# Performance work log

Hardware: AMD Instinct MI355X
Metric: run time of the kernel (lower is better)

Reference implementation:

```python
import jax, jax.numpy as jnp
import numpy as np

T = 2048          # tokens (flattened prefill)
H = 3584          # hidden_size
NH = 16           # num query heads
NKV = 8           # num kv heads
G = NH // NKV     # GQA group size
D = 256           # head_dim
SCALE = 256.0 ** -0.5   # query_pre_attn_scalar ** -0.5
WINDOW = 1024     # sliding_window_size
CAP = 50.0        # logit softcap
BASE = 10000.0    # rope theta
NEG = -1e30


def _rope(x, positions):
    # x: [T, n, D], neox-style rotary over full head_dim
    half = D // 2
    inv_freq = 1.0 / (BASE ** (jnp.arange(0, D, 2, dtype=jnp.float32) / D))  # [half]
    ang = positions.astype(jnp.float32)[:, None] * inv_freq  # [T, half]
    cos = jnp.cos(ang)[:, None, :]  # [T,1,half]
    sin = jnp.sin(ang)[:, None, :]
    x1, x2 = x[..., :half], x[..., half:]
    return jnp.concatenate([x1 * cos - x2 * sin, x2 * cos + x1 * sin], axis=-1)


def setup_inputs() -> dict:
    key = jax.random.key(0)
    ks = jax.random.split(key, 5)
    s = 0.02
    return {
        "hidden_states": jax.random.normal(ks[0], (T, H), dtype=jnp.float32),
        "Wq": jax.random.normal(ks[1], (H, NH * D), dtype=jnp.float32) * s,
        "Wk": jax.random.normal(ks[2], (H, NKV * D), dtype=jnp.float32) * s,
        "Wv": jax.random.normal(ks[3], (H, NKV * D), dtype=jnp.float32) * s,
        "Wo": jax.random.normal(ks[4], (NH * D, H), dtype=jnp.float32) * s,
        "positions": jnp.arange(T, dtype=jnp.int32),
    }


def reference(hidden_states, Wq, Wk, Wv, Wo, positions):
    q = (hidden_states @ Wq).reshape(T, NH, D)
    k = (hidden_states @ Wk).reshape(T, NKV, D)
    v = (hidden_states @ Wv).reshape(T, NKV, D)
    q = _rope(q, positions)
    k = _rope(k, positions)

    # GQA attention: group query heads over kv heads
    qg = (q * SCALE).reshape(T, NKV, G, D)
    scores = jnp.einsum('qhgd,khd->hgqk', qg, k)  # [NKV,G,T,T]
    scores = CAP * jnp.tanh(scores / CAP)         # logit softcap

    i = jnp.arange(T)[:, None]
    j = jnp.arange(T)[None, :]
    mask = (j <= i) & (i - j < WINDOW)            # causal + sliding window
    scores = jnp.where(mask, scores, NEG)

    p = jax.nn.softmax(scores, axis=-1)
    o = jnp.einsum('hgqk,khd->qhgd', p, v).reshape(T, NH * D)
    return o @ Wo
```

## Files before the change

### kernel.cpp

```cpp
#include <hip/hip_runtime.h>
#include <math.h>

typedef __attribute__((ext_vector_type(8))) __bf16 bf16x8;
typedef __attribute__((ext_vector_type(4))) __bf16 bf16x4;
typedef __attribute__((ext_vector_type(4))) float f32x4;

#define TSEQ 2048
#define HDIM 3584
#define NQH  16
#define NKVH 8
#define DH   256
#define WIN  1024
#define QKD  (NQH * DH)
#define KVD  (NKVH * DH)
#define QLD  8256
#define OLD  4160
#define WOLD 4160
#define VLD  2112

#define MFMA __builtin_amdgcn_mfma_f32_16x16x32_bf16

__device__ __forceinline__ void gload_lds16(const void* g, void* l) {
  __builtin_amdgcn_global_load_lds(
      (const __attribute__((address_space(1))) void*)g,
      (__attribute__((address_space(3))) void*)l, 16, 0, 0);
}


__global__ void cvt_bf16_kernel(const float* __restrict__ in,
                                __bf16* __restrict__ out, long n) {
  long i = ((long)blockIdx.x * blockDim.x + threadIdx.x) * 4;
  if (i >= n) return;
  float4 v = *reinterpret_cast<const float4*>(in + i);
  bf16x4 o4;
  o4.x = (__bf16)v.x; o4.y = (__bf16)v.y; o4.z = (__bf16)v.z; o4.w = (__bf16)v.w;
  *reinterpret_cast<bf16x4*>(out + i) = o4;
}

__global__ void transpose_all_kernel(const float* __restrict__ Wq,
                                     const float* __restrict__ Wk,
                                     const float* __restrict__ Wv,
                                     const float* __restrict__ Wo,
                                     __bf16* __restrict__ WqT,
                                     __bf16* __restrict__ WkT,
                                     __bf16* __restrict__ WvT,
                                     __bf16* __restrict__ WoT) {
  __shared__ float tile[64][65];
  int id = blockIdx.x;
  const float* src; __bf16* dst; int R, C, ldo;
  if (id < 3584)      { src = Wq; dst = WqT; R = HDIM; C = QKD; ldo = HDIM; }
  else if (id < 5376) { id -= 3584; src = Wk; dst = WkT; R = HDIM; C = KVD; ldo = HDIM; }
  else if (id < 7168) { id -= 5376; src = Wv; dst = WvT; R = HDIM; C = KVD; ldo = HDIM; }
  else                { id -= 7168; src = Wo; dst = WoT; R = QKD; C = HDIM; ldo = WOLD; }
  const int nbx = C >> 6;
  const int c0 = (id % nbx) * 64, r0 = (id / nbx) * 64;
  const int tid = threadIdx.x;
#pragma unroll
  for (int it = 0; it < 4; ++it) {
    int f = tid + it * 256;
    int row = f >> 4, c4 = (f & 15) * 4;
    float4 v = *reinterpret_cast<const float4*>(&src[(size_t)(r0 + row) * C + c0 + c4]);
    tile[row][c4] = v.x; tile[row][c4 + 1] = v.y;
    tile[row][c4 + 2] = v.z; tile[row][c4 + 3] = v.w;
  }
  __syncthreads();
#pragma unroll
  for (int it = 0; it < 2; ++it) {
    int s = tid + it * 256;
    int oc = s >> 3, rb = (s & 7) * 8;
    bf16x8 o8;
#pragma unroll
    for (int j = 0; j < 8; ++j) o8[j] = (__bf16)tile[rb + j][oc];
    *reinterpret_cast<bf16x8*>(&dst[(size_t)(c0 + oc) * ldo + r0 + rb]) = o8;
  }
}

__global__ void transpose_bf16_kernel(const __bf16* __restrict__ in,
                                      __bf16* __restrict__ out, int ldin, int ldout) {
  __shared__ __bf16 tile[32][33];
  const int tx = threadIdx.x, ty = threadIdx.y;
  const int c0 = blockIdx.x * 32, r0 = blockIdx.y * 32;
#pragma unroll
  for (int i = 0; i < 4; ++i)
    tile[ty + i * 8][tx] = in[(size_t)(r0 + ty + i * 8) * ldin + (c0 + tx)];
  __syncthreads();
#pragma unroll
  for (int i = 0; i < 4; ++i)
    out[(size_t)(c0 + ty + i * 8) * ldout + (r0 + tx)] = tile[tx][ty + i * 8];
}

__global__ void rope_table_kernel(const int* __restrict__ positions,
                                  float* __restrict__ ct,
                                  float* __restrict__ st) {
  int i = blockIdx.x * blockDim.x + threadIdx.x;
  if (i >= TSEQ * 128) return;
  int t = i >> 7, j = i & 127;
  float invf = (float)exp((double)(-2 * j) * (9.210340371976184 / 256.0));
  float ang = (float)positions[t] * invf;
  ct[i] = cosf(ang);
  st[i] = sinf(ang);
}

__global__ void rope_qk_kernel(__bf16* __restrict__ qkv,
                               const float* __restrict__ ct,
                               const float* __restrict__ st) {
  int i = blockIdx.x * blockDim.x + threadIdx.x;
  int jg = (i & 15) * 8;
  int th = i >> 4;
  int t = th / 24;
  int hh = th - t * 24;
  float scale = (hh < 16) ? 0.0625f : 1.0f;
  size_t base = (size_t)t * QLD + ((hh < 16) ? hh * DH : QKD + (hh - 16) * DH) + jg;
  bf16x8 x1 = *reinterpret_cast<const bf16x8*>(qkv + base);
  bf16x8 x2 = *reinterpret_cast<const bf16x8*>(qkv + base + 128);
  const float* cp = ct + (t << 7) + jg;
  const float* sp = st + (t << 7) + jg;
  bf16x8 o1, o2;
#pragma unroll
  for (int e = 0; e < 8; ++e) {
    float c = cp[e], s = sp[e];
    float a = (float)x1[e], b = (float)x2[e];
    o1[e] = (__bf16)((a * c - b * s) * scale);
    o2[e] = (__bf16)((b * c + a * s) * scale);
  }
  *reinterpret_cast<bf16x8*>(qkv + base) = o1;
  *reinterpret_cast<bf16x8*>(qkv + base + 128) = o2;
}


__device__ __forceinline__ void stage_half(const __bf16* __restrict__ gbase,
                                           int row0, int ldg, int k0,
                                           __bf16* lds_half, int tid) {
  const int lane = tid & 63;
  const int w = tid >> 6;
  const int lr = lane >> 3;
  const int swzcol = ((lane & 7) ^ lr) << 3;
  const __bf16* g = gbase + (size_t)(row0 + w * 8 + lr) * ldg + k0 + swzcol;
  __bf16* l = lds_half + w * 512;
  gload_lds16(g, l);
  gload_lds16(g + (size_t)64 * ldg, l + 4096);
}

#define BAR __builtin_amdgcn_s_barrier()

#define RD_A(DST, BASE, MO)                                         \
  _Pragma("unroll")                                                 \
  for (int m_ = 0; m_ < 4; ++m_) {                                  \
    const __bf16* p_ = (BASE) + (((MO) + m_) * 16 + l15) * 64;      \
    DST[m_][0] = *(const bf16x8*)(p_ + kxa);                        \
    DST[m_][1] = *(const bf16x8*)(p_ + kxb);                        \
  }

#define RD_B(DST, BASE, NO)                                         \
  _Pragma("unroll")                                                 \
  for (int n_ = 0; n_ < 2; ++n_) {                                  \
    const __bf16* p_ = (BASE) + (bro + ((NO) + n_) * 16 + l15) * 64;\
    DST[n_][0] = *(const bf16x8*)(p_ + kxa);                        \
    DST[n_][1] = *(const bf16x8*)(p_ + kxb);                        \
  }

#define MQUAD(AF, BF, MO, NO)                                          \
  __builtin_amdgcn_s_setprio(1);                                       \
  _Pragma("unroll")                                                    \
  for (int m_ = 0; m_ < 4; ++m_)                                       \
    _Pragma("unroll")                                                  \
    for (int n_ = 0; n_ < 2; ++n_) {                                   \
      acc[(MO) + m_][(NO) + n_] =                                      \
          MFMA(AF[m_][0], BF[n_][0], acc[(MO) + m_][(NO) + n_], 0, 0, 0); \
      acc[(MO) + m_][(NO) + n_] =                                      \
          MFMA(AF[m_][1], BF[n_][1], acc[(MO) + m_][(NO) + n_], 0, 0, 0); \
    }                                                                  \
  __builtin_amdgcn_s_setprio(0);

__global__ __launch_bounds__(512, 2) void gemm256_kernel(
    const __bf16* __restrict__ A, const __bf16* __restrict__ B,
    __bf16* __restrict__ C, int lda, int Klen, int ldc, int nrc) {
  __shared__ __bf16 lds[2][2][2][8192];

  const int nwg = gridDim.x;
  const int per = nwg >> 3;
  const int wg = (blockIdx.x & 7) * per + (blockIdx.x >> 3);
  const int rem = wg % nrc;
  const int row0 = (rem & 7) * 256;
  const int col0 = (rem >> 3) * 256;
  __bf16* Cs = C;

  const int tid = threadIdx.x;
  const int lane = tid & 63, w = tid >> 6;
  const int wr = w >> 2, wc = w & 3;
  const int l15 = lane & 15, lg = lane >> 4;
  const int kxa = (lg * 8) ^ ((lane & 7) << 3);
  const int kxb = (32 + lg * 8) ^ ((lane & 7) << 3);
  const int bro = (wc & 1) * 64;

  const __bf16* Ablk = A + (size_t)row0 * lda;
  const __bf16* Bblk = B + (size_t)col0 * lda;

  const __bf16* Ae = &lds[0][0][wr][0];
  const __bf16* Be = &lds[0][1][wc >> 1][0];
  const __bf16* Ao = &lds[1][0][wr][0];
  const __bf16* Bo = &lds[1][1][wc >> 1][0];

  f32x4 acc[8][4] = {};
  const int NT = Klen >> 6;
  const int NI = NT >> 1;

  stage_half(Ablk, 0,   lda, 0,  &lds[0][0][0][0], tid);
  stage_half(Ablk, 128, lda, 0,  &lds[0][0][1][0], tid);
  stage_half(Bblk, 0,   lda, 0,  &lds[0][1][0][0], tid);
  stage_half(Bblk, 128, lda, 0,  &lds[0][1][1][0], tid);
  stage_half(Ablk, 0,   lda, 64, &lds[1][0][0][0], tid);
  stage_half(Ablk, 128, lda, 64, &lds[1][0][1][0], tid);
  asm volatile("s_waitcnt vmcnt(4)" ::: "memory");
  BAR;

  bf16x8 a03[4][2], a47[4][2], b01[2][2], b23[2][2];

  for (int j = 0; j < NI; ++j) {
    const int e = 2 * j, o = 2 * j + 1;
    const bool last = (j == NI - 1);

    RD_A(a03, Ae, 0);
    RD_B(b01, Be, 0);
    stage_half(Bblk, 0, lda, o * 64, &lds[1][1][0][0], tid);
    asm volatile("s_waitcnt lgkmcnt(8)" ::: "memory");
    BAR; MQUAD(a03, b01, 0, 0); BAR;

    RD_A(a47, Ae, 4);
    stage_half(Bblk, 128, lda, o * 64, &lds[1][1][1][0], tid);
    BAR; MQUAD(a47, b01, 4, 0); BAR;

    RD_B(b23, Be, 2);
    if (!last) stage_half(Ablk, 0, lda, (e + 2) * 64, &lds[0][0][0][0], tid);
    BAR; MQUAD(a47, b23, 4, 2); BAR;

    if (!last) {
      stage_half(Ablk, 128, lda, (e + 2) * 64, &lds[0][0][1][0], tid);
      asm volatile("s_waitcnt vmcnt(4)" ::: "memory");
    } else {
      asm volatile("s_waitcnt vmcnt(0)" ::: "memory");
    }
    BAR; MQUAD(a03, b23, 0, 2); BAR;

    RD_A(a03, Ao, 0);
    RD_B(b01, Bo, 0);
    if (!last) stage_half(Bblk, 0, lda, (e + 2) * 64, &lds[0][1][0][0], tid);
    asm volatile("s_waitcnt lgkmcnt(8)" ::: "memory");
    BAR; MQUAD(a03, b01, 0, 0); BAR;

    RD_A(a47, Ao, 4);
    if (!last) stage_half(Bblk, 128, lda, (e + 2) * 64, &lds[0][1][1][0], tid);
    BAR; MQUAD(a47, b01, 4, 0); BAR;

    RD_B(b23, Bo, 2);
    if (!last) stage_half(Ablk, 0, lda, (o + 2) * 64, &lds[1][0][0][0], tid);
    BAR; MQUAD(a47, b23, 4, 2); BAR;

    if (!last) {
      stage_half(Ablk, 128, lda, (o + 2) * 64, &lds[1][0][1][0], tid);
      asm volatile("s_waitcnt vmcnt(4)" ::: "memory");
    }
    BAR; MQUAD(a03, b23, 0, 2); BAR;
  }

#pragma unroll
  for (int m = 0; m < 8; ++m)
#pragma unroll
    for (int n = 0; n < 4; ++n)
#pragma unroll
      for (int r = 0; r < 4; ++r) {
        int row = row0 + wr * 128 + m * 16 + lg * 4 + r;
        int col = col0 + wc * 64 + n * 16 + l15;
        Cs[(size_t)row * ldc + col] = (__bf16)acc[m][n][r];
      }
}

__global__ __launch_bounds__(512, 1) void gemm128_kernel(
    const __bf16* __restrict__ A, const __bf16* __restrict__ B,
    float* __restrict__ C, int lda, int Klen, int ldc) {
  __shared__ __bf16 lds[2][3][8192];

  const int per = gridDim.x >> 3;
  const int wg = (blockIdx.x & 7) * per + (blockIdx.x >> 3);
  const int row0 = (wg & 15) * 128;
  const int col0 = (wg >> 4) * 256;

  const int tid = threadIdx.x;
  const int lane = tid & 63, w = tid >> 6;
  const int wr = w >> 2, wc = w & 3;
  const int l15 = lane & 15, lg = lane >> 4;
  const int kxa = (lg * 8) ^ ((lane & 7) << 3);
  const int kxb = (32 + lg * 8) ^ ((lane & 7) << 3);
  const int bro = (wc & 1) * 64;

  const __bf16* Ablk = A + (size_t)row0 * lda;
  const __bf16* Bblk = B + (size_t)col0 * lda;

  f32x4 acc[4][4] = {};
  const int NT = Klen >> 6;

  stage_half(Ablk, 0,   lda, 0,  &lds[0][0][0], tid);
  stage_half(Bblk, 0,   lda, 0,  &lds[0][1][0], tid);
  stage_half(Bblk, 128, lda, 0,  &lds[0][2][0], tid);
  stage_half(Ablk, 0,   lda, 64, &lds[1][0][0], tid);
  asm volatile("s_waitcnt vmcnt(2)" ::: "memory");
  BAR;

  bf16x8 a03[4][2], b01[2][2], b23[2][2];

  for (int t = 0; t < NT; ++t) {
    const int cur = t & 1, nxt = cur ^ 1;
    const __bf16* Ah = &lds[cur][0][0];
    const __bf16* Bh = &lds[cur][1 + (wc >> 1)][0];

    {
      const int MO = wr * 4;
#pragma unroll
      for (int m_ = 0; m_ < 4; ++m_) {
        const __bf16* p_ = Ah + ((MO + m_) * 16 + l15) * 64;
        a03[m_][0] = *(const bf16x8*)(p_ + kxa);
        a03[m_][1] = *(const bf16x8*)(p_ + kxb);
      }
    }
    RD_B(b01, Bh, 0);
    RD_B(b23, Bh, 2);

    if (t + 1 < NT) {
      stage_half(Bblk, 0,   lda, (t + 1) * 64, &lds[nxt][1][0], tid);
      stage_half(Bblk, 128, lda, (t + 1) * 64, &lds[nxt][2][0], tid);
    }

    asm volatile("s_waitcnt lgkmcnt(0)" ::: "memory");
    BAR;
    if (t + 2 < NT) stage_half(Ablk, 0, lda, (t + 2) * 64, &lds[cur][0][0], tid);

    __builtin_amdgcn_s_setprio(1);
#pragma unroll
    for (int m_ = 0; m_ < 4; ++m_) {
#pragma unroll
      for (int n_ = 0; n_ < 2; ++n_) {
        acc[m_][n_] = MFMA(a03[m_][0], b01[n_][0], acc[m_][n_], 0, 0, 0);
        acc[m_][n_] = MFMA(a03[m_][1], b01[n_][1], acc[m_][n_], 0, 0, 0);
        acc[m_][n_ + 2] = MFMA(a03[m_][0], b23[n_][0], acc[m_][n_ + 2], 0, 0, 0);
        acc[m_][n_ + 2] = MFMA(a03[m_][1], b23[n_][1], acc[m_][n_ + 2], 0, 0, 0);
      }
    }
    __builtin_amdgcn_s_setprio(0);

    if (t + 2 < NT) {
      asm volatile("s_waitcnt vmcnt(2)" ::: "memory");
    } else {
      asm volatile("s_waitcnt vmcnt(0)" ::: "memory");
    }
    BAR;
  }

#pragma unroll
  for (int m = 0; m < 4; ++m)
#pragma unroll
    for (int n = 0; n < 4; ++n)
#pragma unroll
      for (int r = 0; r < 4; ++r) {
        int row = row0 + wr * 64 + m * 16 + lg * 4 + r;
        int col = col0 + wc * 64 + n * 16 + l15;
        C[(size_t)row * ldc + col] = acc[m][n][r];
      }
}


__device__ __forceinline__ void attn_stage(const __bf16* __restrict__ kg,
                                           const __bf16* __restrict__ vg,
                                           __bf16* Kd, __bf16* Vd, int tid) {
#pragma unroll
  for (int i = 0; i < 8; ++i) {
    int c = tid + i * 256;
    int krow = c >> 5, kslot = c & 31;
    gload_lds16(kg + (size_t)krow * QLD + ((kslot ^ (krow & 7)) * 8), Kd + c * 8);
    int vrow = c >> 3, vslot = c & 7;
    gload_lds16(vg + (size_t)vrow * VLD + ((vslot ^ (vrow & 7)) * 8), Vd + c * 8);
  }
}

__global__ __launch_bounds__(256, 2) void attn_kernel(
    const __bf16* __restrict__ q, const __bf16* __restrict__ k,
    const __bf16* __restrict__ vt, __bf16* __restrict__ o) {
  __shared__ __bf16 Klds[64][256];
  __shared__ __bf16 Vlds[256][64];
  __shared__ __bf16 Plds[4][16][72];

  const int tid = threadIdx.x;
  const int wave = tid >> 6;
  const int lane = tid & 63;
  const int l16 = lane & 15;
  const int lg = lane >> 4;
  const int h = blockIdx.x;
  const int qh = 2 * h + (blockIdx.y & 1);
  const int q0 = (31 - (int)(blockIdx.y >> 1)) << 6;
  const int qr = q0 + wave * 16;

  const __bf16* kg0 = k + (size_t)h * DH;
  const __bf16* vg0 = vt + (size_t)(h * DH) * VLD;

  int t_lo = q0 - (WIN - 1);
  if (t_lo < 0) t_lo = 0;
  t_lo &= ~63;
  const int NTile = ((q0 - t_lo) >> 6) + 1;

  bf16x8 qf[8];
  {
    const __bf16* qp = q + (size_t)(qr + l16) * QLD + qh * DH + lg * 8;
#pragma unroll
    for (int ds = 0; ds < 8; ++ds)
      qf[ds] = *reinterpret_cast<const bf16x8*>(qp + ds * 32);
  }

  f32x4 accO[16] = {};
  float l_run[4] = {0.f, 0.f, 0.f, 0.f};

  for (int it = 0; it < NTile; ++it) {
    const int t0 = t_lo + it * 64;

    attn_stage(kg0 + (size_t)t0 * QLD, vg0 + t0, &Klds[0][0], &Vlds[0][0], tid);
    asm volatile("s_waitcnt vmcnt(0)" ::: "memory");
    __builtin_amdgcn_s_barrier();

    f32x4 accS[4] = {};
    __builtin_amdgcn_s_setprio(1);
#pragma unroll
    for (int ds = 0; ds < 8; ++ds)
#pragma unroll
      for (int nt = 0; nt < 4; ++nt) {
        int row = nt * 16 + l16;
        int slot = (4 * ds + lg) ^ (l16 & 7);
        bf16x8 kf = *reinterpret_cast<const bf16x8*>(&Klds[0][0] + row * 256 + slot * 8);
        accS[nt] = MFMA(qf[ds], kf, accS[nt], 0, 0, 0);
      }
    __builtin_amdgcn_s_setprio(0);

    float rs[4] = {0.f, 0.f, 0.f, 0.f};
#pragma unroll
    for (int nt = 0; nt < 4; ++nt) {
      int key = t0 + nt * 16 + l16;
#pragma unroll
      for (int r = 0; r < 4; ++r) {
        int row = qr + lg * 4 + r;
        float t = __expf(accS[nt][r] * 0.04f);
        float p = __expf(-100.0f / (t + 1.0f));
        bool valid = (key <= row) && (row - key < WIN);
        p = valid ? p : 0.f;
        rs[r] += p;
        Plds[wave][lg * 4 + r][nt * 16 + l16] = (__bf16)p;
      }
    }
#pragma unroll
    for (int off = 1; off < 16; off <<= 1)
#pragma unroll
      for (int r = 0; r < 4; ++r)
        rs[r] += __shfl_xor(rs[r], off);
#pragma unroll
    for (int r = 0; r < 4; ++r)
      l_run[r] += rs[r];

    __builtin_amdgcn_s_setprio(1);
#pragma unroll
    for (int ks = 0; ks < 2; ++ks) {
      bf16x8 pa = *reinterpret_cast<const bf16x8*>(&Plds[wave][l16][ks * 32 + lg * 8]);
#pragma unroll
      for (int nt2 = 0; nt2 < 16; ++nt2) {
        int row = nt2 * 16 + l16;
        int slot = (4 * ks + lg) ^ (l16 & 7);
        bf16x8 vb = *reinterpret_cast<const bf16x8*>(&Vlds[0][0] + row * 64 + slot * 8);
        accO[nt2] = MFMA(pa, vb, accO[nt2], 0, 0, 0);
      }
    }
    __builtin_amdgcn_s_setprio(0);
    __builtin_amdgcn_s_barrier();
  }

#pragma unroll
  for (int r = 0; r < 4; ++r) {
    float inv_l = 1.f / l_run[r];
    int row = qr + lg * 4 + r;
#pragma unroll
    for (int nt2 = 0; nt2 < 16; ++nt2)
      o[(size_t)row * OLD + qh * DH + nt2 * 16 + l16] = (__bf16)(accO[nt2][r] * inv_l);
  }
}


extern "C" void kernel_launch(void* const* d_in, const int* in_sizes, int n_in,
                              void* d_out, int out_size, void* d_ws, size_t ws_size,
                              hipStream_t stream) {
  const float* hs = (const float*)d_in[0];
  const float* Wq = (const float*)d_in[1];
  const float* Wk = (const float*)d_in[2];
  const float* Wv = (const float*)d_in[3];
  const float* Wo = (const float*)d_in[4];
  const int* positions = (const int*)d_in[5];
  float* out = (float*)d_out;

  char* ws = (char*)d_ws;
  const size_t SZ_HS  = (size_t)TSEQ * HDIM * 2;
  const size_t SZ_WQT = (size_t)QKD * HDIM * 2;
  const size_t SZ_WKT = (size_t)KVD * HDIM * 2;
  const size_t SZ_WOT = (size_t)HDIM * WOLD * 2;
  const size_t SZ_QKV = (size_t)TSEQ * QLD * 2;
  const size_t SZ_O   = (size_t)TSEQ * OLD * 2;
  const size_t SZ_TBL = (size_t)TSEQ * 128 * 4;

  __bf16* hs_bf = (__bf16*)ws; ws += SZ_HS;
  __bf16* WqT   = (__bf16*)ws; ws += SZ_WQT;
  __bf16* WkT   = (__bf16*)ws; ws += SZ_WKT;
  __bf16* WvT   = (__bf16*)ws; ws += SZ_WKT;
  __bf16* WoT   = (__bf16*)ws; ws += SZ_WOT;
  __bf16* qkv   = (__bf16*)ws; ws += SZ_QKV;
  __bf16* o_bf  = (__bf16*)ws; ws += SZ_O;
  float*  cost  = (float*)ws;  ws += SZ_TBL;
  float*  sint  = (float*)ws;  ws += SZ_TBL;
  __bf16* vt_bf = hs_bf;
  if ((size_t)(ws - (char*)d_ws) > ws_size) return;

  cvt_bf16_kernel<<<(TSEQ * HDIM) / 1024, 256, 0, stream>>>(hs, hs_bf, (long)TSEQ * HDIM);
  transpose_all_kernel<<<10752, 256, 0, stream>>>(Wq, Wk, Wv, Wo, WqT, WkT, WvT, WoT);
  rope_table_kernel<<<(TSEQ * 128) / 256, 256, 0, stream>>>(positions, cost, sint);

  gemm256_kernel<<<256, 512, 0, stream>>>(hs_bf, WqT, qkv, HDIM, HDIM, QLD, 256);

  rope_qk_kernel<<<(TSEQ * 24 * 16) / 256, 256, 0, stream>>>(qkv, cost, sint);
  transpose_bf16_kernel<<<dim3(KVD / 32, TSEQ / 32), dim3(32, 8), 0, stream>>>(qkv + QKD + KVD, vt_bf, QLD, VLD);

  attn_kernel<<<dim3(NKVH, 64), 256, 0, stream>>>(qkv, qkv + QKD, vt_bf, o_bf);

  gemm128_kernel<<<224, 512, 0, stream>>>(o_bf, WoT, out, OLD, QKD, HDIM);
}
```

Baseline: 305.8 us.

## Replace 256x256 QKV GEMM with 256x128 tile, BK=32 kernel over 512 blocks

Swaps the hand-scheduled 256x256 tile, BK=64 QKV projection GEMM for a simpler 256x128 tile kernel with a K-step of 32 and a double-buffered, XOR-swizzled LDS layout. The grid grows from 256 to 512 workgroups. This should fill the CUs better and cut per-block register and LDS pressure, at the cost of more global traffic per FLOP and more barriers per K. It also gives the V transpose its own workspace buffer instead of aliasing hs_bf.

```diff
diff --git a/kernel.cpp b/kernel.cpp
--- a/kernel.cpp
+++ b/kernel.cpp
@@ -127,6 +127,108 @@
   *reinterpret_cast<bf16x8*>(qkv + base + 128) = o2;
 }
 
+#define BAR __builtin_amdgcn_s_barrier()
+
+
+__device__ __forceinline__ void stage32(const __bf16* __restrict__ gbase,
+                                        int row0, int lda, int k0,
+                                        __bf16* lds_half, int tid) {
+  const int row = tid >> 2;
+  const int slot = tid & 3;
+  const __bf16* g = gbase + (size_t)(row0 + row) * lda + k0 +
+                    ((slot ^ ((row >> 1) & 3)) << 3);
+  gload_lds16(g, lds_half + tid * 8);
+}
+
+__global__ __launch_bounds__(512, 2) void gemmqkv_kernel(
+    const __bf16* __restrict__ A, const __bf16* __restrict__ B,
+    __bf16* __restrict__ C, int lda, int Klen, int ldc) {
+  __shared__ __bf16 lds[2][3][4096];
+
+  const int per = gridDim.x >> 3;
+  const int wg = (blockIdx.x & 7) * per + (blockIdx.x >> 3);
+  const int row0 = (wg & 7) * 256;
+  const int col0 = (wg >> 3) * 128;
+
+  const int tid = threadIdx.x;
+  const int lane = tid & 63, w = tid >> 6;
+  const int wr = w >> 1, wc = w & 1;
+  const int l15 = lane & 15, lg = lane >> 4;
+
+  const __bf16* Ablk = A + (size_t)row0 * lda;
+  const __bf16* Bblk = B + (size_t)col0 * lda;
+
+  f32x4 acc[4][4] = {};
+  const int NT = Klen >> 5;
+
+  int aoff[4], boff[4];
+#pragma unroll
+  for (int m = 0; m < 4; ++m) {
+    int r = wr * 64 + m * 16 + l15;
+    int rl = r & 127;
+    aoff[m] = (r >> 7) * 4096 + rl * 32 + ((lg ^ ((rl >> 1) & 3)) << 3);
+  }
+#pragma unroll
+  for (int n = 0; n < 4; ++n) {
+    int r = wc * 64 + n * 16 + l15;
+    boff[n] = 8192 + r * 32 + ((lg ^ ((r >> 1) & 3)) << 3);
+  }
+
+  stage32(Ablk, 0,   lda, 0,  &lds[0][0][0], tid);
+  stage32(Ablk, 128, lda, 0,  &lds[0][1][0], tid);
+  stage32(Bblk, 0,   lda, 0,  &lds[0][2][0], tid);
+  stage32(Ablk, 0,   lda, 32, &lds[1][0][0], tid);
+  stage32(Ablk, 128, lda, 32, &lds[1][1][0], tid);
+  asm volatile("s_waitcnt vmcnt(2)" ::: "memory");
+  BAR;
+
+  for (int t = 0; t < NT; ++t) {
+    const int cur = t & 1, nxt = cur ^ 1;
+    const __bf16* base = &lds[cur][0][0];
+
+    bf16x8 a[4], b[4];
+#pragma unroll
+    for (int m = 0; m < 4; ++m) a[m] = *(const bf16x8*)(base + aoff[m]);
+#pragma unroll
+    for (int n = 0; n < 4; ++n) b[n] = *(const bf16x8*)(base + boff[n]);
+
+    if (t + 1 < NT) stage32(Bblk, 0, lda, (t + 1) * 32, &lds[nxt][2][0], tid);
+
+    asm volatile("s_waitcnt lgkmcnt(0)" ::: "memory");
+    BAR;
+    if (t + 2 < NT) {
+      stage32(Ablk, 0,   lda, (t + 2) * 32, &lds[cur][0][0], tid);
+      stage32(Ablk, 128, lda, (t + 2) * 32, &lds[cur][1][0], tid);
+    }
+
+    __builtin_amdgcn_s_setprio(1);
+#pragma unroll
+    for (int m = 0; m < 4; ++m)
+#pragma unroll
+      for (int n = 0; n < 4; ++n)
+        acc[m][n] = MFMA(a[m], b[n], acc[m][n], 0, 0, 0);
+    __builtin_amdgcn_s_setprio(0);
+
+    if (t + 2 < NT) {
+      asm volatile("s_waitcnt vmcnt(2)" ::: "memory");
+    } else {
+      asm volatile("s_waitcnt vmcnt(0)" ::: "memory");
+    }
+    BAR;
+  }
+
+#pragma unroll
+  for (int m = 0; m < 4; ++m)
+#pragma unroll
+    for (int n = 0; n < 4; ++n)
+#pragma unroll
+      for (int r = 0; r < 4; ++r) {
+        int row = row0 + wr * 64 + m * 16 + lg * 4 + r;
+        int col = col0 + wc * 64 + n * 16 + l15;
+        C[(size_t)row * ldc + col] = (__bf16)acc[m][n][r];
+      }
+}
+
 
 __device__ __forceinline__ void stage_half(const __bf16* __restrict__ gbase,
                                            int row0, int ldg, int k0,
@@ -141,16 +243,6 @@
   gload_lds16(g + (size_t)64 * ldg, l + 4096);
 }
 
-#define BAR __builtin_amdgcn_s_barrier()
-
-#define RD_A(DST, BASE, MO)                                         \
-  _Pragma("unroll")                                                 \
-  for (int m_ = 0; m_ < 4; ++m_) {                                  \
-    const __bf16* p_ = (BASE) + (((MO) + m_) * 16 + l15) * 64;      \
-    DST[m_][0] = *(const bf16x8*)(p_ + kxa);                        \
-    DST[m_][1] = *(const bf16x8*)(p_ + kxb);                        \
-  }
-
 #define RD_B(DST, BASE, NO)                                         \
   _Pragma("unroll")                                                 \
   for (int n_ = 0; n_ < 2; ++n_) {                                  \
@@ -158,122 +250,6 @@
     DST[n_][0] = *(const bf16x8*)(p_ + kxa);                        \
     DST[n_][1] = *(const bf16x8*)(p_ + kxb);                        \
   }
-
-#define MQUAD(AF, BF, MO, NO)                                          \
-  __builtin_amdgcn_s_setprio(1);                                       \
-  _Pragma("unroll")                                                    \
-  for (int m_ = 0; m_ < 4; ++m_)                                       \
-    _Pragma("unroll")                                                  \
-    for (int n_ = 0; n_ < 2; ++n_) {                                   \
-      acc[(MO) + m_][(NO) + n_] =                                      \
-          MFMA(AF[m_][0], BF[n_][0], acc[(MO) + m_][(NO) + n_], 0, 0, 0); \
-      acc[(MO) + m_][(NO) + n_] =                                      \
-          MFMA(AF[m_][1], BF[n_][1], acc[(MO) + m_][(NO) + n_], 0, 0, 0); \
-    }                                                                  \
-  __builtin_amdgcn_s_setprio(0);
-
-__global__ __launch_bounds__(512, 2) void gemm256_kernel(
-    const __bf16* __restrict__ A, const __bf16* __restrict__ B,
-    __bf16* __restrict__ C, int lda, int Klen, int ldc, int nrc) {
-  __shared__ __bf16 lds[2][2][2][8192];
-
-  const int nwg = gridDim.x;
-  const int per = nwg >> 3;
-  const int wg = (blockIdx.x & 7) * per + (blockIdx.x >> 3);
-  const int rem = wg % nrc;
-  const int row0 = (rem & 7) * 256;
-  const int col0 = (rem >> 3) * 256;
-  __bf16* Cs = C;
-
-  const int tid = threadIdx.x;
-  const int lane = tid & 63, w = tid >> 6;
-  const int wr = w >> 2, wc = w & 3;
-  const int l15 = lane & 15, lg = lane >> 4;
-  const int kxa = (lg * 8) ^ ((lane & 7) << 3);
-  const int kxb = (32 + lg * 8) ^ ((lane & 7) << 3);
-  const int bro = (wc & 1) * 64;
-
-  const __bf16* Ablk = A + (size_t)row0 * lda;
-  const __bf16* Bblk = B + (size_t)col0 * lda;
-
-  const __bf16* Ae = &lds[0][0][wr][0];
-  const __bf16* Be = &lds[0][1][wc >> 1][0];
-  const __bf16* Ao = &lds[1][0][wr][0];
-  const __bf16* Bo = &lds[1][1][wc >> 1][0];
-
-  f32x4 acc[8][4] = {};
-  const int NT = Klen >> 6;
-  const int NI = NT >> 1;
-
-  stage_half(Ablk, 0,   lda, 0,  &lds[0][0][0][0], tid);
-  stage_half(Ablk, 128, lda, 0,  &lds[0][0][1][0], tid);
-  stage_half(Bblk, 0,   lda, 0,  &lds[0][1][0][0], tid);
-  stage_half(Bblk, 128, lda, 0,  &lds[0][1][1][0], tid);
-  stage_half(Ablk, 0,   lda, 64, &lds[1][0][0][0], tid);
-  stage_half(Ablk, 128, lda, 64, &lds[1][0][1][0], tid);
-  asm volatile("s_waitcnt vmcnt(4)" ::: "memory");
-  BAR;
-
-  bf16x8 a03[4][2], a47[4][2], b01[2][2], b23[2][2];
-
-  for (int j = 0; j < NI; ++j) {
-    const int e = 2 * j, o = 2 * j + 1;
-    const bool last = (j == NI - 1);
-
-    RD_A(a03, Ae, 0);
-    RD_B(b01, Be, 0);
-    stage_half(Bblk, 0, lda, o * 64, &lds[1][1][0][0], tid);
-    asm volatile("s_waitcnt lgkmcnt(8)" ::: "memory");
-    BAR; MQUAD(a03, b01, 0, 0); BAR;
-
-    RD_A(a47, Ae, 4);
-    stage_half(Bblk, 128, lda, o * 64, &lds[1][1][1][0], tid);
-    BAR; MQUAD(a47, b01, 4, 0); BAR;
-
-    RD_B(b23, Be, 2);
-    if (!last) stage_half(Ablk, 0, lda, (e + 2) * 64, &lds[0][0][0][0], tid);
-    BAR; MQUAD(a47, b23, 4, 2); BAR;
-
-    if (!last) {
-      stage_half(Ablk, 128, lda, (e + 2) * 64, &lds[0][0][1][0], tid);
-      asm volatile("s_waitcnt vmcnt(4)" ::: "memory");
-    } else {
-      asm volatile("s_waitcnt vmcnt(0)" ::: "memory");
-    }
-    BAR; MQUAD(a03, b23, 0, 2); BAR;
-
-    RD_A(a03, Ao, 0);
-    RD_B(b01, Bo, 0);
-    if (!last) stage_half(Bblk, 0, lda, (e + 2) * 64, &lds[0][1][0][0], tid);
-    asm volatile("s_waitcnt lgkmcnt(8)" ::: "memory");
-    BAR; MQUAD(a03, b01, 0, 0); BAR;
-
-    RD_A(a47, Ao, 4);
-    if (!last) stage_half(Bblk, 128, lda, (e + 2) * 64, &lds[0][1][1][0], tid);
-    BAR; MQUAD(a47, b01, 4, 0); BAR;
-
-    RD_B(b23, Bo, 2);
-    if (!last) stage_half(Ablk, 0, lda, (o + 2) * 64, &lds[1][0][0][0], tid);
-    BAR; MQUAD(a47, b23, 4, 2); BAR;
-
-    if (!last) {
-      stage_half(Ablk, 128, lda, (o + 2) * 64, &lds[1][0][1][0], tid);
-      asm volatile("s_waitcnt vmcnt(4)" ::: "memory");
-    }
-    BAR; MQUAD(a03, b23, 0, 2); BAR;
-  }
-
-#pragma unroll
-  for (int m = 0; m < 8; ++m)
-#pragma unroll
-    for (int n = 0; n < 4; ++n)
-#pragma unroll
-      for (int r = 0; r < 4; ++r) {
-        int row = row0 + wr * 128 + m * 16 + lg * 4 + r;
-        int col = col0 + wc * 64 + n * 16 + l15;
-        Cs[(size_t)row * ldc + col] = (__bf16)acc[m][n][r];
-      }
-}
 
 __global__ __launch_bounds__(512, 1) void gemm128_kernel(
     const __bf16* __restrict__ A, const __bf16* __restrict__ B,
@@ -506,6 +482,7 @@
   const size_t SZ_WOT = (size_t)HDIM * WOLD * 2;
   const size_t SZ_QKV = (size_t)TSEQ * QLD * 2;
   const size_t SZ_O   = (size_t)TSEQ * OLD * 2;
+  const size_t SZ_VT  = (size_t)KVD * VLD * 2;
   const size_t SZ_TBL = (size_t)TSEQ * 128 * 4;
 
   __bf16* hs_bf = (__bf16*)ws; ws += SZ_HS;
@@ -515,16 +492,16 @@
   __bf16* WoT   = (__bf16*)ws; ws += SZ_WOT;
   __bf16* qkv   = (__bf16*)ws; ws += SZ_QKV;
   __bf16* o_bf  = (__bf16*)ws; ws += SZ_O;
+  __bf16* vt_bf = (__bf16*)ws; ws += SZ_VT;
   float*  cost  = (float*)ws;  ws += SZ_TBL;
   float*  sint  = (float*)ws;  ws += SZ_TBL;
-  __bf16* vt_bf = hs_bf;
   if ((size_t)(ws - (char*)d_ws) > ws_size) return;
 
   cvt_bf16_kernel<<<(TSEQ * HDIM) / 1024, 256, 0, stream>>>(hs, hs_bf, (long)TSEQ * HDIM);
   transpose_all_kernel<<<10752, 256, 0, stream>>>(Wq, Wk, Wv, Wo, WqT, WkT, WvT, WoT);
   rope_table_kernel<<<(TSEQ * 128) / 256, 256, 0, stream>>>(positions, cost, sint);
 
-  gemm256_kernel<<<256, 512, 0, stream>>>(hs_bf, WqT, qkv, HDIM, HDIM, QLD, 256);
+  gemmqkv_kernel<<<512, 512, 0, stream>>>(hs_bf, WqT, qkv, HDIM, HDIM, QLD);
 
   rope_qk_kernel<<<(TSEQ * 24 * 16) / 256, 256, 0, stream>>>(qkv, cost, sint);
   transpose_bf16_kernel<<<dim3(KVD / 32, TSEQ / 32), dim3(32, 8), 0, stream>>>(qkv + QKD + KVD, vt_bf, QLD, VLD);
```

Measured after the change: 335.4 us. +9.6%, slower.
